# Kernel optimization log

Measured on AMD Instinct MI355X. Metric: run time of the kernel, lower is better.

Reference implementation:

```python
import jax, jax.numpy as jnp
import numpy as np

B, N, IN_DIM, OUT_DIM, H = 4, 2048, 128, 128, 4
NEG_SLOPE = 0.2


def setup_inputs() -> dict:
    key = jax.random.key(0)
    ks = jax.random.split(key, 6)
    # Xavier-ish scaling for stable softmax logits
    node_features = jax.random.normal(ks[0], (B, N, IN_DIM), dtype=jnp.float32)
    adjacency = jax.random.randint(ks[1], (B, N, N), 0, 2, dtype=jnp.int32)
    W = jax.random.normal(ks[2], (H, IN_DIM, OUT_DIM), dtype=jnp.float32) / np.sqrt(IN_DIM)
    a = jax.random.normal(ks[3], (H, 2 * OUT_DIM), dtype=jnp.float32) / np.sqrt(2 * OUT_DIM)
    out_proj_w = jax.random.normal(ks[4], (H * OUT_DIM, OUT_DIM), dtype=jnp.float32) / np.sqrt(H * OUT_DIM)
    out_proj_b = jax.random.normal(ks[5], (OUT_DIM,), dtype=jnp.float32) * 0.01
    return {"node_features": node_features, "adjacency": adjacency, "W": W,
            "a": a, "out_proj_w": out_proj_w, "out_proj_b": out_proj_b}


def reference(node_features, adjacency, W, a, out_proj_w, out_proj_b):
    D = W.shape[-1]
    # Per-head projection: h[b,h,n,o]
    h = jnp.einsum('bni,hio->bhno', node_features, W)
    # Additive attention score a^T [h_i || h_j] decomposed into src+dst parts
    # (exact since the score Linear has no bias).
    s = jnp.einsum('bhno,ho->bhn', h, a[:, :D])   # contribution of h_i
    d = jnp.einsum('bhno,ho->bhn', h, a[:, D:])   # contribution of h_j
    e = jax.nn.leaky_relu(s[..., :, None] + d[..., None, :], NEG_SLOPE)  # [B,H,N,N]
    e = jnp.where(adjacency[:, None, :, :] == 0, -jnp.inf, e)
    alpha = jax.nn.softmax(e, axis=-1)                                   # [B,H,N,N]
    out = jnp.einsum('bhnm,bhmo->bhno', alpha, h)                        # [B,H,N,D]
    b, nh, n, _ = out.shape
    cat = out.transpose(0, 2, 1, 3).reshape(b, n, nh * D)                # concat heads
    output = cat @ out_proj_w + out_proj_b                               # [B,N,D]
    return output, alpha
```

## Files before the change

### kernel.cpp

```cpp
#include <hip/hip_runtime.h>
#include <hip/hip_bf16.h>

#define BB 4
#define NN 2048
#define DD 128
#define HH 4
#define LOG2E 1.4426950408889634f
#define NEG_BIG (-1e30f)

typedef __attribute__((ext_vector_type(8))) short bf16x8;
typedef __attribute__((ext_vector_type(4))) short bf16x4;
typedef __attribute__((ext_vector_type(4))) float f32x4;

__device__ __forceinline__ unsigned short f2bf(float f) {
    union { float f; unsigned int u; } v; v.f = f;
    unsigned int r = v.u + 0x7FFF + ((v.u >> 16) & 1);
    return (unsigned short)(r >> 16);
}

__global__ __launch_bounds__(128) void k_wvec(const float* __restrict__ W,
                                              const float* __restrict__ a,
                                              float* __restrict__ wsv,
                                              float* __restrict__ wdv) {
    int h = blockIdx.x;
    int i = threadIdx.x;
    const float* Wr  = W + (h * DD + i) * DD;
    const float* as_ = a + h * 2 * DD;
    const float* ad_ = as_ + DD;
    float s = 0.f, d = 0.f;
    for (int o = 0; o < DD; ++o) {
        float w = Wr[o];
        s += w * as_[o];
        d += w * ad_[o];
    }
    wsv[h * DD + i] = s;
    wdv[h * DD + i] = d;
}

__global__ __launch_bounds__(256) void k_h(const float* __restrict__ x,
                                           const float* __restrict__ W,
                                           const float* __restrict__ wsv,
                                           const float* __restrict__ wdv,
                                           unsigned short* __restrict__ hT,
                                           float* __restrict__ s_out,
                                           float* __restrict__ d_out_) {
    __shared__ float xs[32 * 132];
    int tid = threadIdx.x;
    int bh = blockIdx.x / (NN / 32);
    int nb = (blockIdx.x % (NN / 32)) * 32;
    int b = bh >> 2, h = bh & 3;
    for (int idx = tid; idx < 32 * 128; idx += 256) {
        int r = idx >> 7, c = idx & 127;
        xs[r * 132 + c] = x[((size_t)b * NN + nb + r) * DD + c];
    }
    __syncthreads();
    int o = tid & 127, rh = tid >> 7;
    float acc[16];
#pragma unroll
    for (int j = 0; j < 16; ++j) acc[j] = 0.f;
    const float* Wc = W + (size_t)h * DD * DD + o;
    for (int i = 0; i < DD; i += 4) {
        float w0 = Wc[(i + 0) * DD];
        float w1 = Wc[(i + 1) * DD];
        float w2 = Wc[(i + 2) * DD];
        float w3 = Wc[(i + 3) * DD];
#pragma unroll
        for (int j = 0; j < 16; ++j) {
            float4 xq = *(const float4*)&xs[(rh * 16 + j) * 132 + i];
            acc[j] += xq.x * w0 + xq.y * w1 + xq.z * w2 + xq.w * w3;
        }
    }
    bf16x8 p0, p1;
#pragma unroll
    for (int j = 0; j < 8; ++j) { p0[j] = (short)f2bf(acc[j]); p1[j] = (short)f2bf(acc[8 + j]); }
    unsigned short* dst = hT + ((size_t)bh * DD + o) * NN + nb + rh * 16;
    *(bf16x8*)dst = p0;
    *(bf16x8*)(dst + 8) = p1;

    {
        int r = tid >> 3, seg = (tid & 7) * 16;
        const float* wsp = wsv + h * DD + seg;
        const float* wdp = wdv + h * DD + seg;
        float sv = 0.f, dv = 0.f;
#pragma unroll
        for (int j = 0; j < 16; j += 4) {
            float4 xq = *(const float4*)&xs[r * 132 + seg + j];
            float4 wq = *(const float4*)(wsp + j);
            float4 vq = *(const float4*)(wdp + j);
            sv += xq.x * wq.x + xq.y * wq.y + xq.z * wq.z + xq.w * wq.w;
            dv += xq.x * vq.x + xq.y * vq.y + xq.z * vq.z + xq.w * vq.w;
        }
#pragma unroll
        for (int off = 1; off < 8; off <<= 1) {
            sv += __shfl_xor(sv, off, 64);
            dv += __shfl_xor(dv, off, 64);
        }
        if ((tid & 7) == 0) {
            s_out[(b * HH + h) * NN + nb + r]  = sv;
            d_out_[(b * HH + h) * NN + nb + r] = dv;
        }
    }
}

__global__ __launch_bounds__(256) void k_dmax(const float* __restrict__ d_,
                                              float* __restrict__ dmax_) {
    __shared__ float red[4];
    int bh = blockIdx.x, tid = threadIdx.x;
    const float4* dp = (const float4*)(d_ + (size_t)bh * NN);
    float4 v0 = dp[tid];
    float4 v1 = dp[256 + tid];
    float m = fmaxf(fmaxf(fmaxf(v0.x, v0.y), fmaxf(v0.z, v0.w)),
                    fmaxf(fmaxf(v1.x, v1.y), fmaxf(v1.z, v1.w)));
#pragma unroll
    for (int off = 32; off >= 1; off >>= 1)
        m = fmaxf(m, __shfl_xor(m, off, 64));
    if ((tid & 63) == 0) red[tid >> 6] = m;
    __syncthreads();
    if (tid == 0)
        dmax_[bh] = fmaxf(fmaxf(red[0], red[1]), fmaxf(red[2], red[3]));
}

struct TileRegs {
    int4   a4[8];
    float4 d4;
    bf16x8 hv[8];
};
struct P1Regs {
    int4   a4[8];
    float4 d4;
};

__device__ __forceinline__ void attn_load_tile(int mb, const int* adj_base,
                                               const float* dg, int ac4,
                                               const unsigned short* hbase,
                                               TileRegs& R) {
#pragma unroll
    for (int p = 0; p < 8; ++p)
        R.a4[p] = *(const int4*)(adj_base + (size_t)(p * 8) * NN + mb);
    R.d4 = *(const float4*)(dg + mb + ac4);
#pragma unroll
    for (int q = 0; q < 8; ++q)
        R.hv[q] = *(const bf16x8*)(hbase + (size_t)(q * 16) * NN + mb);
}

__device__ __forceinline__ void p1_load(int mb, const int* adj_base,
                                        const float* dg, int ac4, P1Regs& R) {
#pragma unroll
    for (int p = 0; p < 8; ++p)
        R.a4[p] = *(const int4*)(adj_base + (size_t)(p * 8) * NN + mb);
    R.d4 = *(const float4*)(dg + mb + ac4);
}

__device__ __forceinline__ void p1_accum(const P1Regs& R, const float (&sreg)[8],
                                         const float (&Mreg)[8], float (&Lp)[8]) {
#pragma unroll
    for (int p = 0; p < 8; ++p) {
        float sn = sreg[p], Mn = Mreg[p];
        float t0 = sn + R.d4.x, t1 = sn + R.d4.y;
        float t2 = sn + R.d4.z, t3 = sn + R.d4.w;
        float v0 = t0 > 0.f ? t0 : 0.2f * t0;
        float v1 = t1 > 0.f ? t1 : 0.2f * t1;
        float v2 = t2 > 0.f ? t2 : 0.2f * t2;
        float v3 = t3 > 0.f ? t3 : 0.2f * t3;
        float e0 = (R.a4[p].x != 0) ? exp2f((v0 - Mn) * LOG2E) : 0.f;
        float e1 = (R.a4[p].y != 0) ? exp2f((v1 - Mn) * LOG2E) : 0.f;
        float e2 = (R.a4[p].z != 0) ? exp2f((v2 - Mn) * LOG2E) : 0.f;
        float e3 = (R.a4[p].w != 0) ? exp2f((v3 - Mn) * LOG2E) : 0.f;
        Lp[p] += (e0 + e1) + (e2 + e3);
    }
}

template <bool WRITE_ALPHA>
__device__ __forceinline__ void attn_tile_body(
    int mb, TileRegs& cur, TileRegs& nxt,
    const int* adj_base, const float* dg, int ac4,
    const unsigned short* hbase,
    unsigned short* al_lds, unsigned short* hT_lds,
    const float (&sreg)[8], const float (&Mreg)[8], const float (&Lin)[8],
    float* alpha_base, int ar0, int hrow0, int hbyte,
    int w, int col, int quad, f32x4 (&acc)[8])
{
#pragma unroll
    for (int p = 0; p < 8; ++p) {
        int row = p * 8 + ar0;
        float sn = sreg[p], Mn = Mreg[p], Li = Lin[p];
        float t0 = sn + cur.d4.x, t1 = sn + cur.d4.y;
        float t2 = sn + cur.d4.z, t3 = sn + cur.d4.w;
        float v0 = t0 > 0.f ? t0 : 0.2f * t0;
        float v1 = t1 > 0.f ? t1 : 0.2f * t1;
        float v2 = t2 > 0.f ? t2 : 0.2f * t2;
        float v3 = t3 > 0.f ? t3 : 0.2f * t3;
        float e0 = (cur.a4[p].x != 0) ? exp2f((v0 - Mn) * LOG2E) * Li : 0.f;
        float e1 = (cur.a4[p].y != 0) ? exp2f((v1 - Mn) * LOG2E) * Li : 0.f;
        float e2 = (cur.a4[p].z != 0) ? exp2f((v2 - Mn) * LOG2E) * Li : 0.f;
        float e3 = (cur.a4[p].w != 0) ? exp2f((v3 - Mn) * LOG2E) * Li : 0.f;
        bf16x4 pk;
        pk[0] = (short)f2bf(e0); pk[1] = (short)f2bf(e1);
        pk[2] = (short)f2bf(e2); pk[3] = (short)f2bf(e3);
        int abyte = (ac4 * 2) ^ ((row & 15) << 4);
        *(bf16x4*)&al_lds[row * 128 + (abyte >> 1)] = pk;
        if (WRITE_ALPHA) {
            float4 ev; ev.x = e0; ev.y = e1; ev.z = e2; ev.w = e3;
            *(float4*)(alpha_base + (size_t)(p * 8) * NN + mb) = ev;
        }
    }
#pragma unroll
    for (int q = 0; q < 8; ++q)
        *(bf16x8*)&hT_lds[(q * 16 + hrow0) * 128 + (hbyte >> 1)] = cur.hv[q];

    attn_load_tile((mb + 128) & (NN - 1), adj_base, dg, ac4, hbase, nxt);

    __syncthreads();
#pragma unroll
    for (int k = 0; k < 4; ++k) {
        int cbyte = (k * 64 + quad * 16) ^ (col << 4);
        bf16x8 af = *(const bf16x8*)&al_lds[(w * 16 + col) * 128 + (cbyte >> 1)];
#pragma unroll
        for (int ot = 0; ot < 8; ++ot) {
            bf16x8 bfv = *(const bf16x8*)&hT_lds[(ot * 16 + col) * 128 + (cbyte >> 1)];
            acc[ot] = __builtin_amdgcn_mfma_f32_16x16x32_bf16(af, bfv, acc[ot], 0, 0, 0);
        }
    }
    __syncthreads();
}

template <bool WRITE_ALPHA>
__global__ __launch_bounds__(256) void k_attn_mfma(const int* __restrict__ adj,
                                                   const float* __restrict__ s_in,
                                                   const float* __restrict__ d_in_,
                                                   const float* __restrict__ dmax_,
                                                   const unsigned short* __restrict__ hT,
                                                   float* __restrict__ out_scr,
                                                   float* __restrict__ alpha_out,
                                                   float* __restrict__ Li_out) {
    __shared__ unsigned short al_lds[64 * 128];
    __shared__ unsigned short hT_lds[128 * 128];
    int tid = threadIdx.x;
    int bid = (int)(blockIdx.x & 7) * 64 + (int)(blockIdx.x >> 3);
    int bh = bid >> 5;
    int nb = (bid & 31) * 64;
    int b = bh >> 2;

    int ar0 = tid >> 5;
    int ac4 = (tid & 31) * 4;
    const int* adj_base = adj + ((size_t)b * NN + nb + ar0) * NN + ac4;
    float* alpha_base = WRITE_ALPHA
        ? alpha_out + ((size_t)bh * NN + nb + ar0) * NN + ac4 : nullptr;
    const float* dg = d_in_ + (size_t)bh * NN;

    float dmx = dmax_[bh];
    float sreg[8], Mreg[8];
#pragma unroll
    for (int p = 0; p < 8; ++p) {
        sreg[p] = s_in[bh * NN + nb + p * 8 + ar0];
        float t = sreg[p] + dmx;
        Mreg[p] = t > 0.f ? t : 0.2f * t;
    }

    float Lp[8];
#pragma unroll
    for (int p = 0; p < 8; ++p) Lp[p] = 0.f;
    {
        P1Regs A0, A1;
        p1_load(0, adj_base, dg, ac4, A0);
        for (int mb = 0; mb < NN; mb += 256) {
            p1_load(mb + 128, adj_base, dg, ac4, A1);
            p1_accum(A0, sreg, Mreg, Lp);
            p1_load((mb + 256) & (NN - 1), adj_base, dg, ac4, A0);
            p1_accum(A1, sreg, Mreg, Lp);
        }
    }
#pragma unroll
    for (int off = 16; off >= 1; off >>= 1)
#pragma unroll
        for (int p = 0; p < 8; ++p)
            Lp[p] += __shfl_xor(Lp[p], off, 64);
    float Lin[8];
#pragma unroll
    for (int p = 0; p < 8; ++p) Lin[p] = Lp[p] > 0.f ? 1.f / Lp[p] : 0.f;
    if (!WRITE_ALPHA && (tid & 31) == 0) {
#pragma unroll
        for (int p = 0; p < 8; ++p)
            Li_out[bh * NN + nb + p * 8 + ar0] = Lin[p];
    }

    int hrow0 = tid >> 4;
    int hcolu = (tid & 15) * 8;
    const unsigned short* hbase = hT + ((size_t)bh * DD + hrow0) * NN + hcolu;
    int hbyte = (hcolu * 2) ^ (hrow0 << 4);
    int l = tid & 63, w = tid >> 6, col = l & 15, quad = l >> 4;

    f32x4 acc[8];
#pragma unroll
    for (int ot = 0; ot < 8; ++ot) acc[ot] = (f32x4){0.f, 0.f, 0.f, 0.f};

    TileRegs R0, R1;
    attn_load_tile(0, adj_base, dg, ac4, hbase, R0);

    for (int mb = 0; mb < NN; mb += 256) {
        attn_tile_body<WRITE_ALPHA>(mb, R0, R1, adj_base, dg, ac4, hbase,
                                    al_lds, hT_lds, sreg, Mreg, Lin,
                                    alpha_base, ar0, hrow0, hbyte,
                                    w, col, quad, acc);
        attn_tile_body<WRITE_ALPHA>(mb + 128, R1, R0, adj_base, dg, ac4, hbase,
                                    al_lds, hT_lds, sreg, Mreg, Lin,
                                    alpha_base, ar0, hrow0, hbyte,
                                    w, col, quad, acc);
    }
#pragma unroll
    for (int ot = 0; ot < 8; ++ot)
#pragma unroll
        for (int r = 0; r < 4; ++r)
            out_scr[((size_t)bh * NN + nb + w * 16 + quad * 4 + r) * DD + ot * 16 + col] =
                acc[ot][r];
}

__global__ __launch_bounds__(256) void k_proj(const float* __restrict__ out_scr,
                                              const float* __restrict__ Wp,
                                              const float* __restrict__ bias,
                                              float* __restrict__ out) {
    __shared__ float cs[16 * 512];
    int tid = threadIdx.x;
    int b  = blockIdx.x / (NN / 16);
    int nb = (blockIdx.x % (NN / 16)) * 16;
    for (int idx = tid; idx < 16 * 512; idx += 256) {
        int r = idx >> 9, c = idx & 511;
        int hh = c >> 7, oo = c & 127;
        cs[idx] = out_scr[((size_t)(b * HH + hh) * NN + nb + r) * DD + oo];
    }
    __syncthreads();
    int o = tid & 63, rg = tid >> 6;
    float bv0 = bias[o], bv1 = bias[o + 64];
    float acc0[4], acc1[4];
#pragma unroll
    for (int j = 0; j < 4; ++j) { acc0[j] = bv0; acc1[j] = bv1; }
    for (int k = 0; k < 512; k += 4) {
        float w00 = Wp[(k + 0) * DD + o], w01 = Wp[(k + 0) * DD + o + 64];
        float w10 = Wp[(k + 1) * DD + o], w11 = Wp[(k + 1) * DD + o + 64];
        float w20 = Wp[(k + 2) * DD + o], w21 = Wp[(k + 2) * DD + o + 64];
        float w30 = Wp[(k + 3) * DD + o], w31 = Wp[(k + 3) * DD + o + 64];
#pragma unroll
        for (int j = 0; j < 4; ++j) {
            float4 cq = *(const float4*)&cs[(rg * 4 + j) * 512 + k];
            acc0[j] += cq.x * w00 + cq.y * w10 + cq.z * w20 + cq.w * w30;
            acc1[j] += cq.x * w01 + cq.y * w11 + cq.z * w21 + cq.w * w31;
        }
    }
#pragma unroll
    for (int j = 0; j < 4; ++j) {
        out[((size_t)b * NN + nb + rg * 4 + j) * DD + o]      = acc0[j];
        out[((size_t)b * NN + nb + rg * 4 + j) * DD + o + 64] = acc1[j];
    }
}

__global__ __launch_bounds__(256) void k_alpha(const int* __restrict__ adj,
                                               const float* __restrict__ s_in,
                                               const float* __restrict__ d_in_,
                                               const float* __restrict__ dmax_,
                                               const float* __restrict__ Li_in,
                                               float* __restrict__ alpha_out) {
    int tid = threadIdx.x;
    int b = blockIdx.x / NN, n = blockIdx.x % NN;
    float sv[4], Mv[4], Lv[4];
#pragma unroll
    for (int h = 0; h < 4; ++h) {
        sv[h] = s_in[(b * HH + h) * NN + n];
        float t = sv[h] + dmax_[b * HH + h];
        Mv[h] = t > 0.f ? t : 0.2f * t;
        Lv[h] = Li_in[(b * HH + h) * NN + n];
    }
    const int* arow = adj + ((size_t)b * NN + n) * NN;
    for (int m = tid; m < NN; m += 256) {
        int av = arow[m];
#pragma unroll
        for (int h = 0; h < 4; ++h) {
            float val = 0.f;
            if (av != 0) {
                float t = sv[h] + d_in_[(b * HH + h) * NN + m];
                float v = t > 0.f ? t : 0.2f * t;
                val = exp2f((v - Mv[h]) * LOG2E) * Lv[h];
            }
            alpha_out[((size_t)(b * HH + h) * NN + n) * NN + m] = val;
        }
    }
}

extern "C" void kernel_launch(void* const* d_in, const int* in_sizes, int n_in,
                              void* d_out, int out_size, void* d_ws, size_t ws_size,
                              hipStream_t stream) {
    const float* x    = (const float*)d_in[0];
    const int*   adj  = (const int*)d_in[1];
    const float* W    = (const float*)d_in[2];
    const float* a    = (const float*)d_in[3];
    const float* Wp   = (const float*)d_in[4];
    const float* bias = (const float*)d_in[5];

    float* out       = (float*)d_out;
    float* alpha_out = out + (size_t)BB * NN * DD;

    float* ws   = (float*)d_ws;
    float* wsv  = ws;
    float* wdv  = wsv + HH * DD;
    float* s_   = wdv + HH * DD;
    float* d_   = s_ + (size_t)BB * HH * NN;
    float* Li_  = d_ + (size_t)BB * HH * NN;
    float* dmax_= Li_ + (size_t)BB * HH * NN;

    const size_t stats_bytes = (2 * HH * DD + 3 * (size_t)BB * HH * NN + 16) * sizeof(float);
    const size_t hT_bytes    = (size_t)BB * HH * NN * DD * sizeof(unsigned short);
    const size_t scr_bytes   = (size_t)BB * HH * NN * DD * sizeof(float);
    const bool fused = ws_size >= stats_bytes + hT_bytes + scr_bytes;

    unsigned short* hT;
    float* out_scr;
    if (fused) {
        hT      = (unsigned short*)((char*)d_ws + stats_bytes);
        out_scr = (float*)((char*)hT + hT_bytes);
    } else {
        hT      = (unsigned short*)alpha_out;
        out_scr = alpha_out + (size_t)BB * HH * NN * DD;
    }

    k_wvec<<<HH, 128, 0, stream>>>(W, a, wsv, wdv);
    k_h<<<BB * HH * (NN / 32), 256, 0, stream>>>(x, W, wsv, wdv, hT, s_, d_);
    k_dmax<<<BB * HH, 256, 0, stream>>>(d_, dmax_);
    if (fused) {
        k_attn_mfma<true><<<BB * HH * (NN / 64), 256, 0, stream>>>(adj, s_, d_, dmax_,
                                                                   hT, out_scr, alpha_out, Li_);
        k_proj<<<BB * (NN / 16), 256, 0, stream>>>(out_scr, Wp, bias, out);
    } else {
        k_attn_mfma<false><<<BB * HH * (NN / 64), 256, 0, stream>>>(adj, s_, d_, dmax_,
                                                                    hT, out_scr, alpha_out, Li_);
        k_proj<<<BB * (NN / 16), 256, 0, stream>>>(out_scr, Wp, bias, out);
        k_alpha<<<BB * NN, 256, 0, stream>>>(adj, s_, d_, dmax_, Li_, alpha_out);
    }
}
```

Before: 454.9 us.

## Compute head projection with fp16 MFMA and restructure attention prefetch

Replaces the scalar FP32 per-head projection kernel with an MFMA fp16 kernel that stages a transposed fp16 copy of W and fp16 x in swizzled LDS. The s/d score vectors move into a separate small kernel. The attention loop now loads h tiles just in time and prefetches only adjacency and d, which cuts register pressure from double-buffered h vectors. This adds an extra launch and fp16 rounding of x and W before the bf16 storage of h.

```diff
diff --git a/kernel.cpp b/kernel.cpp
--- a/kernel.cpp
+++ b/kernel.cpp
@@ -11,6 +11,8 @@
 typedef __attribute__((ext_vector_type(8))) short bf16x8;
 typedef __attribute__((ext_vector_type(4))) short bf16x4;
 typedef __attribute__((ext_vector_type(4))) float f32x4;
+typedef __attribute__((ext_vector_type(8))) _Float16 f16x8;
+typedef __attribute__((ext_vector_type(4))) _Float16 f16x4;
 
 __device__ __forceinline__ unsigned short f2bf(float f) {
     union { float f; unsigned int u; } v; v.f = f;
@@ -18,10 +20,11 @@
     return (unsigned short)(r >> 16);
 }
 
-__global__ __launch_bounds__(128) void k_wvec(const float* __restrict__ W,
+__global__ __launch_bounds__(128) void k_prep(const float* __restrict__ W,
                                               const float* __restrict__ a,
                                               float* __restrict__ wsv,
-                                              float* __restrict__ wdv) {
+                                              float* __restrict__ wdv,
+                                              _Float16* __restrict__ WT16) {
     int h = blockIdx.x;
     int i = threadIdx.x;
     const float* Wr  = W + (h * DD + i) * DD;
@@ -32,74 +35,100 @@
         float w = Wr[o];
         s += w * as_[o];
         d += w * ad_[o];
+        WT16[((size_t)h * DD + o) * DD + i] = (_Float16)w;
     }
     wsv[h * DD + i] = s;
     wdv[h * DD + i] = d;
 }
 
-__global__ __launch_bounds__(256) void k_h(const float* __restrict__ x,
-                                           const float* __restrict__ W,
-                                           const float* __restrict__ wsv,
-                                           const float* __restrict__ wdv,
-                                           unsigned short* __restrict__ hT,
-                                           float* __restrict__ s_out,
-                                           float* __restrict__ d_out_) {
-    __shared__ float xs[32 * 132];
+__global__ __launch_bounds__(256) void k_sd(const float* __restrict__ x,
+                                            const float* __restrict__ wsv,
+                                            const float* __restrict__ wdv,
+                                            float* __restrict__ s_out,
+                                            float* __restrict__ d_out_) {
+    __shared__ float xs[64 * 129];
+    __shared__ float ws[4 * 129], wd[4 * 129];
     int tid = threadIdx.x;
-    int bh = blockIdx.x / (NN / 32);
-    int nb = (blockIdx.x % (NN / 32)) * 32;
+    int b  = blockIdx.x / (NN / 64);
+    int nb = (blockIdx.x % (NN / 64)) * 64;
+    for (int idx = tid; idx < HH * DD; idx += 256) {
+        ws[(idx >> 7) * 129 + (idx & 127)] = wsv[idx];
+        wd[(idx >> 7) * 129 + (idx & 127)] = wdv[idx];
+    }
+    for (int idx = tid; idx < 64 * 128; idx += 256) {
+        int r = idx >> 7, c = idx & 127;
+        xs[r * 129 + c] = x[((size_t)b * NN + nb + r) * DD + c];
+    }
+    __syncthreads();
+    int h = tid & 3, r = tid >> 2;
+    float sv = 0.f, dv = 0.f;
+#pragma unroll 8
+    for (int i = 0; i < DD; ++i) {
+        float xv = xs[r * 129 + i];
+        sv += xv * ws[h * 129 + i];
+        dv += xv * wd[h * 129 + i];
+    }
+    int n = nb + r;
+    s_out[(b * HH + h) * NN + n] = sv;
+    d_out_[(b * HH + h) * NN + n] = dv;
+}
+
+__global__ __launch_bounds__(256) void k_h_mfma(const float* __restrict__ x,
+                                                const _Float16* __restrict__ WT16,
+                                                unsigned short* __restrict__ hT) {
+    __shared__ unsigned short wt_lds[128 * 128];
+    __shared__ unsigned short x_lds[64 * 128];
+    int tid = threadIdx.x;
+    int bh = blockIdx.x >> 5;
+    int nb = (blockIdx.x & 31) * 64;
     int b = bh >> 2, h = bh & 3;
-    for (int idx = tid; idx < 32 * 128; idx += 256) {
-        int r = idx >> 7, c = idx & 127;
-        xs[r * 132 + c] = x[((size_t)b * NN + nb + r) * DD + c];
-    }
-    __syncthreads();
-    int o = tid & 127, rh = tid >> 7;
-    float acc[16];
-#pragma unroll
-    for (int j = 0; j < 16; ++j) acc[j] = 0.f;
-    const float* Wc = W + (size_t)h * DD * DD + o;
-    for (int i = 0; i < DD; i += 4) {
-        float w0 = Wc[(i + 0) * DD];
-        float w1 = Wc[(i + 1) * DD];
-        float w2 = Wc[(i + 2) * DD];
-        float w3 = Wc[(i + 3) * DD];
-#pragma unroll
-        for (int j = 0; j < 16; ++j) {
-            float4 xq = *(const float4*)&xs[(rh * 16 + j) * 132 + i];
-            acc[j] += xq.x * w0 + xq.y * w1 + xq.z * w2 + xq.w * w3;
-        }
-    }
-    bf16x8 p0, p1;
-#pragma unroll
-    for (int j = 0; j < 8; ++j) { p0[j] = (short)f2bf(acc[j]); p1[j] = (short)f2bf(acc[8 + j]); }
-    unsigned short* dst = hT + ((size_t)bh * DD + o) * NN + nb + rh * 16;
-    *(bf16x8*)dst = p0;
-    *(bf16x8*)(dst + 8) = p1;
 
     {
-        int r = tid >> 3, seg = (tid & 7) * 16;
-        const float* wsp = wsv + h * DD + seg;
-        const float* wdp = wdv + h * DD + seg;
-        float sv = 0.f, dv = 0.f;
-#pragma unroll
-        for (int j = 0; j < 16; j += 4) {
-            float4 xq = *(const float4*)&xs[r * 132 + seg + j];
-            float4 wq = *(const float4*)(wsp + j);
-            float4 vq = *(const float4*)(wdp + j);
-            sv += xq.x * wq.x + xq.y * wq.y + xq.z * wq.z + xq.w * wq.w;
-            dv += xq.x * vq.x + xq.y * vq.y + xq.z * vq.z + xq.w * vq.w;
-        }
-#pragma unroll
-        for (int off = 1; off < 8; off <<= 1) {
-            sv += __shfl_xor(sv, off, 64);
-            dv += __shfl_xor(dv, off, 64);
-        }
-        if ((tid & 7) == 0) {
-            s_out[(b * HH + h) * NN + nb + r]  = sv;
-            d_out_[(b * HH + h) * NN + nb + r] = dv;
-        }
-    }
+        int o = tid >> 1, ihalf = (tid & 1) * 64;
+        const _Float16* src = WT16 + ((size_t)h * DD + o) * DD + ihalf;
+#pragma unroll
+        for (int q = 0; q < 8; ++q) {
+            f16x8 v = *(const f16x8*)(src + q * 8);
+            int byte = ((ihalf + q * 8) * 2) ^ ((o & 15) << 4);
+            *(f16x8*)&wt_lds[o * 128 + (byte >> 1)] = v;
+        }
+    }
+    {
+        int n = tid >> 2, iseg = (tid & 3) * 32;
+        const float* src = x + ((size_t)b * NN + nb + n) * DD + iseg;
+#pragma unroll
+        for (int q = 0; q < 8; ++q) {
+            float4 v = *(const float4*)(src + q * 4);
+            f16x4 p;
+            p[0] = (_Float16)v.x; p[1] = (_Float16)v.y;
+            p[2] = (_Float16)v.z; p[3] = (_Float16)v.w;
+            int byte = ((iseg + q * 4) * 2) ^ ((n & 15) << 4);
+            *(f16x4*)&x_lds[n * 128 + (byte >> 1)] = p;
+        }
+    }
+    __syncthreads();
+
+    int l = tid & 63, w = tid >> 6, col = l & 15, quad = l >> 4;
+    f32x4 acc[8];
+#pragma unroll
+    for (int ot = 0; ot < 8; ++ot) acc[ot] = (f32x4){0.f, 0.f, 0.f, 0.f};
+#pragma unroll
+    for (int k = 0; k < 4; ++k) {
+        int cbyte = (k * 64 + quad * 16) ^ (col << 4);
+        f16x8 bv = *(const f16x8*)&x_lds[(w * 16 + col) * 128 + (cbyte >> 1)];
+#pragma unroll
+        for (int ot = 0; ot < 8; ++ot) {
+            f16x8 av = *(const f16x8*)&wt_lds[(ot * 16 + col) * 128 + (cbyte >> 1)];
+            acc[ot] = __builtin_amdgcn_mfma_f32_16x16x32_f16(av, bv, acc[ot], 0, 0, 0);
+        }
+    }
+    unsigned short* base = hT + (size_t)bh * DD * NN;
+#pragma unroll
+    for (int ot = 0; ot < 8; ++ot)
+#pragma unroll
+        for (int r = 0; r < 4; ++r)
+            base[(size_t)(ot * 16 + quad * 4 + r) * NN + nb + w * 16 + col] =
+                f2bf(acc[ot][r]);
 }
 
 __global__ __launch_bounds__(256) void k_dmax(const float* __restrict__ d_,
@@ -120,38 +149,20 @@
         dmax_[bh] = fmaxf(fmaxf(red[0], red[1]), fmaxf(red[2], red[3]));
 }
 
-struct TileRegs {
-    int4   a4[8];
-    float4 d4;
-    bf16x8 hv[8];
-};
-struct P1Regs {
+struct AdjD {
     int4   a4[8];
     float4 d4;
 };
 
-__device__ __forceinline__ void attn_load_tile(int mb, const int* adj_base,
-                                               const float* dg, int ac4,
-                                               const unsigned short* hbase,
-                                               TileRegs& R) {
+__device__ __forceinline__ void adjd_load(int mb, const int* adj_base,
+                                          const float* dg, int ac4, AdjD& R) {
 #pragma unroll
     for (int p = 0; p < 8; ++p)
         R.a4[p] = *(const int4*)(adj_base + (size_t)(p * 8) * NN + mb);
     R.d4 = *(const float4*)(dg + mb + ac4);
-#pragma unroll
-    for (int q = 0; q < 8; ++q)
-        R.hv[q] = *(const bf16x8*)(hbase + (size_t)(q * 16) * NN + mb);
-}
-
-__device__ __forceinline__ void p1_load(int mb, const int* adj_base,
-                                        const float* dg, int ac4, P1Regs& R) {
-#pragma unroll
-    for (int p = 0; p < 8; ++p)
-        R.a4[p] = *(const int4*)(adj_base + (size_t)(p * 8) * NN + mb);
-    R.d4 = *(const float4*)(dg + mb + ac4);
-}
-
-__device__ __forceinline__ void p1_accum(const P1Regs& R, const float (&sreg)[8],
+}
+
+__device__ __forceinline__ void p1_accum(const AdjD& R, const float (&sreg)[8],
                                          const float (&Mreg)[8], float (&Lp)[8]) {
 #pragma unroll
     for (int p = 0; p < 8; ++p) {
@@ -172,7 +183,7 @@
 
 template <bool WRITE_ALPHA>
 __device__ __forceinline__ void attn_tile_body(
-    int mb, TileRegs& cur, TileRegs& nxt,
+    int mb, AdjD& cur, AdjD& nxt,
     const int* adj_base, const float* dg, int ac4,
     const unsigned short* hbase,
     unsigned short* al_lds, unsigned short* hT_lds,
@@ -180,6 +191,12 @@
     float* alpha_base, int ar0, int hrow0, int hbyte,
     int w, int col, int quad, f32x4 (&acc)[8])
 {
+    bf16x8 hv[8];
+#pragma unroll
+    for (int q = 0; q < 8; ++q)
+        hv[q] = *(const bf16x8*)(hbase + (size_t)(q * 16) * NN + mb);
+    adjd_load((mb + 128) & (NN - 1), adj_base, dg, ac4, nxt);
+
 #pragma unroll
     for (int p = 0; p < 8; ++p) {
         int row = p * 8 + ar0;
@@ -206,9 +223,7 @@
     }
 #pragma unroll
     for (int q = 0; q < 8; ++q)
-        *(bf16x8*)&hT_lds[(q * 16 + hrow0) * 128 + (hbyte >> 1)] = cur.hv[q];
-
-    attn_load_tile((mb + 128) & (NN - 1), adj_base, dg, ac4, hbase, nxt);
+        *(bf16x8*)&hT_lds[(q * 16 + hrow0) * 128 + (hbyte >> 1)] = hv[q];
 
     __syncthreads();
 #pragma unroll
@@ -261,12 +276,12 @@
 #pragma unroll
     for (int p = 0; p < 8; ++p) Lp[p] = 0.f;
     {
-        P1Regs A0, A1;
-        p1_load(0, adj_base, dg, ac4, A0);
+        AdjD A0, A1;
+        adjd_load(0, adj_base, dg, ac4, A0);
         for (int mb = 0; mb < NN; mb += 256) {
-            p1_load(mb + 128, adj_base, dg, ac4, A1);
+            adjd_load(mb + 128, adj_base, dg, ac4, A1);
             p1_accum(A0, sreg, Mreg, Lp);
-            p1_load((mb + 256) & (NN - 1), adj_base, dg, ac4, A0);
+            adjd_load((mb + 256) & (NN - 1), adj_base, dg, ac4, A0);
             p1_accum(A1, sreg, Mreg, Lp);
         }
     }
@@ -294,15 +309,15 @@
 #pragma unroll
     for (int ot = 0; ot < 8; ++ot) acc[ot] = (f32x4){0.f, 0.f, 0.f, 0.f};
 
-    TileRegs R0, R1;
-    attn_load_tile(0, adj_base, dg, ac4, hbase, R0);
+    AdjD A0, A1;
+    adjd_load(0, adj_base, dg, ac4, A0);
 
     for (int mb = 0; mb < NN; mb += 256) {
-        attn_tile_body<WRITE_ALPHA>(mb, R0, R1, adj_base, dg, ac4, hbase,
+        attn_tile_body<WRITE_ALPHA>(mb, A0, A1, adj_base, dg, ac4, hbase,
                                     al_lds, hT_lds, sreg, Mreg, Lin,
                                     alpha_base, ar0, hrow0, hbyte,
                                     w, col, quad, acc);
-        attn_tile_body<WRITE_ALPHA>(mb + 128, R1, R0, adj_base, dg, ac4, hbase,
+        attn_tile_body<WRITE_ALPHA>(mb + 128, A1, A0, adj_base, dg, ac4, hbase,
                                     al_lds, hT_lds, sreg, Mreg, Lin,
                                     alpha_base, ar0, hrow0, hbyte,
                                     w, col, quad, acc);
@@ -398,15 +413,17 @@
     float* out       = (float*)d_out;
     float* alpha_out = out + (size_t)BB * NN * DD;
 
-    float* ws   = (float*)d_ws;
-    float* wsv  = ws;
-    float* wdv  = wsv + HH * DD;
-    float* s_   = wdv + HH * DD;
-    float* d_   = s_ + (size_t)BB * HH * NN;
-    float* Li_  = d_ + (size_t)BB * HH * NN;
-    float* dmax_= Li_ + (size_t)BB * HH * NN;
-
-    const size_t stats_bytes = (2 * HH * DD + 3 * (size_t)BB * HH * NN + 16) * sizeof(float);
+    float* ws    = (float*)d_ws;
+    float* wsv   = ws;
+    float* wdv   = wsv + HH * DD;
+    float* s_    = wdv + HH * DD;
+    float* d_    = s_ + (size_t)BB * HH * NN;
+    float* Li_   = d_ + (size_t)BB * HH * NN;
+    float* dmax_ = Li_ + (size_t)BB * HH * NN;
+    _Float16* WT16 = (_Float16*)(dmax_ + 16);
+
+    const size_t stats_bytes = (2 * HH * DD + 3 * (size_t)BB * HH * NN + 16) * sizeof(float)
+                             + (size_t)HH * DD * DD * sizeof(_Float16);
     const size_t hT_bytes    = (size_t)BB * HH * NN * DD * sizeof(unsigned short);
     const size_t scr_bytes   = (size_t)BB * HH * NN * DD * sizeof(float);
     const bool fused = ws_size >= stats_bytes + hT_bytes + scr_bytes;
@@ -421,8 +438,9 @@
         out_scr = alpha_out + (size_t)BB * HH * NN * DD;
     }
 
-    k_wvec<<<HH, 128, 0, stream>>>(W, a, wsv, wdv);
-    k_h<<<BB * HH * (NN / 32), 256, 0, stream>>>(x, W, wsv, wdv, hT, s_, d_);
+    k_prep<<<HH, 128, 0, stream>>>(W, a, wsv, wdv, WT16);
+    k_sd<<<BB * NN / 64, 256, 0, stream>>>(x, wsv, wdv, s_, d_);
+    k_h_mfma<<<BB * HH * (NN / 64), 256, 0, stream>>>(x, WT16, hT);
     k_dmax<<<BB * HH, 256, 0, stream>>>(d_, dmax_);
     if (fused) {
         k_attn_mfma<true><<<BB * HH * (NN / 64), 256, 0, stream>>>(adj, s_, d_, dmax_,
```

Result: faster. 444.7 us (-2.2%).
